# Performance work log

Hardware: AMD Instinct MI355X
Metric: run time of the kernel (lower is better)

## Reference

```python
import jax, jax.numpy as jnp
import numpy as np
import math

N = 4096; NFEAT = 512; HID = 128; H = 4; DH = HID // H; NC = 16; FF = 2 * HID


def _ln(x, g, b):
    m = jnp.mean(x, -1, keepdims=True)
    v = jnp.var(x, -1, keepdims=True)
    return (x - m) / jnp.sqrt(v + 1e-5) * g + b


def setup_inputs() -> dict:
    key = jax.random.key(0)
    ks = jax.random.split(key, 16)

    def w(k, shape):
        s = 1.0 / np.sqrt(shape[0])
        return jax.random.uniform(k, shape, jnp.float32, -s, s)

    inp = {}
    inp['e'] = jax.random.uniform(ks[0], (N,), jnp.float32, 0.0, 2.0)  # eigenvalues
    inp['u'] = jax.random.normal(ks[1], (N, N), jnp.float32) / np.sqrt(N)  # eigenvectors
    inp['x'] = jax.random.normal(ks[2], (N, NFEAT), jnp.float32)
    # feat_encoder: Linear(nfeat,hid) -> ReLU -> Linear(hid,nclass)
    inp['fe_w1'] = w(ks[3], (NFEAT, HID)); inp['fe_b1'] = jnp.zeros((HID,), jnp.float32)
    inp['fe_w2'] = w(ks[4], (HID, NC));    inp['fe_b2'] = jnp.zeros((NC,), jnp.float32)
    # eig_w: Linear(hid+1, hid)
    inp['ew_w'] = w(ks[5], (HID + 1, HID)); inp['ew_b'] = jnp.zeros((HID,), jnp.float32)
    inp['ln1_g'] = jnp.ones((HID,), jnp.float32); inp['ln1_b'] = jnp.zeros((HID,), jnp.float32)
    # custom MHA projections
    inp['wq'] = w(ks[6], (HID, HID)); inp['bq'] = jnp.zeros((HID,), jnp.float32)
    inp['wk'] = w(ks[7], (HID, HID)); inp['bk'] = jnp.zeros((HID,), jnp.float32)
    inp['wv'] = w(ks[8], (HID, HID)); inp['bv'] = jnp.zeros((HID,), jnp.float32)
    inp['wo'] = w(ks[9], (HID, HID)); inp['bo'] = jnp.zeros((HID,), jnp.float32)
    inp['ln2_g'] = jnp.ones((HID,), jnp.float32); inp['ln2_b'] = jnp.zeros((HID,), jnp.float32)
    # FFN with GELU
    inp['ffn_w1'] = w(ks[10], (HID, FF)); inp['ffn_b1'] = jnp.zeros((FF,), jnp.float32)
    inp['ffn_w2'] = w(ks[11], (FF, HID)); inp['ffn_b2'] = jnp.zeros((HID,), jnp.float32)
    # decoder: Linear(hid, nheads)
    inp['dec_w'] = w(ks[12], (HID, H)); inp['dec_b'] = jnp.zeros((H,), jnp.float32)
    # SpecLayer weight (norm='none' -> ones, [1, nheads+1, nclass])
    inp['spec_w'] = jnp.ones((1, H + 1, NC), jnp.float32)
    return inp


def reference(e, u, x, fe_w1, fe_b1, fe_w2, fe_b2, ew_w, ew_b, ln1_g, ln1_b,
              wq, bq, wk, bk, wv, bv, wo, bo, ln2_g, ln2_b,
              ffn_w1, ffn_b1, ffn_w2, ffn_b2, dec_w, dec_b, spec_w):
    n = e.shape[0]
    # feat_encoder (norm='none' path), dropout is identity at p=0
    h = jax.nn.relu(x @ fe_w1 + fe_b1) @ fe_w2 + fe_b2  # [N, NC]
    # SineEncoding
    div = jnp.exp(jnp.arange(0, HID, 2, dtype=jnp.float32) * (-math.log(10000.0) / HID))  # [HID/2]
    pe = (e * 100.0)[:, None] * div                     # [N, HID/2]
    sc = jnp.concatenate([jnp.sin(pe), jnp.cos(pe)], axis=1)   # [N, HID] (sin_cos_encoding)
    eeig = jnp.concatenate([e[:, None], sc], axis=1)           # [N, HID+1]
    eigw = eeig @ ew_w + ew_b                                  # [N, HID]
    # Custom multi-head attention with dot-product relative-position bias
    m = _ln(eigw, ln1_g, ln1_b)
    q = (m @ wq + bq).reshape(n, H, DH).transpose(1, 0, 2)     # [H, N, DH]
    k = (m @ wk + bk).reshape(n, H, DH).transpose(1, 0, 2)
    v = (m @ wv + bv).reshape(n, H, DH).transpose(1, 0, 2)
    rel = sc @ sc.T                                            # [N, N]
    scale = 1.0 / math.sqrt(DH)
    scores = jnp.einsum('hnd,hmd->hnm', q, k) * scale + rel[None] * scale  # [H, N, N]
    attn = jax.nn.softmax(scores, axis=-1)
    out = jnp.einsum('hnm,hmd->hnd', attn, v).transpose(1, 0, 2).reshape(n, HID)
    out = out @ wo + bo
    eig = eigw + out
    f = _ln(eig, ln2_g, ln2_b)
    f = jax.nn.gelu(f @ ffn_w1 + ffn_b1, approximate=False) @ ffn_w2 + ffn_b2
    eig = eig + f
    new_e = eig @ dec_w + dec_b                                # [N, H]
    # Spectral propagation (single SpecLayer, norm='none')
    utx = u.T @ h                                              # [N, NC]
    scaled = new_e.T[:, :, None] * utx[None]                   # [H, N, NC]
    props = jnp.einsum('nm,hmc->hnc', u, scaled)               # [H, N, NC]
    bf = jnp.concatenate([h[:, None, :], props.transpose(1, 0, 2)], axis=1)  # [N, H+1, NC]
    return jnp.sum(bf * spec_w, axis=1)                        # [N, NC]
```

## Files before the change

kernel.cpp:

```cpp
#include <hip/hip_runtime.h>
#include <math.h>

#define N 4096
#define NFEAT 512
#define HID 128
#define NHEAD 4
#define DH 32
#define NC 16
#define FF 256
#define NSPLIT 32
#define NCHUNK 8

typedef _Float16 f16;
typedef unsigned int uint;
typedef _Float16 f16x8 __attribute__((ext_vector_type(8)));
typedef _Float16 f16x2 __attribute__((ext_vector_type(2)));
typedef float f32x16 __attribute__((ext_vector_type(16)));

#define SCALE 0.17677669529663687f
#define LOG2E 1.44269504088896f
#define SH2   (-14.0f * 1.44269504088896f)

__global__ __launch_bounds__(256) void k_feat(const float* __restrict__ x,
    const float* __restrict__ w1, const float* __restrict__ b1,
    const float* __restrict__ w2, const float* __restrict__ b2,
    float* __restrict__ h) {
  __shared__ float xs[8][NFEAT];
  __shared__ float h1s[8][HID];
  int r0 = blockIdx.x * 8, tid = threadIdx.x;
  for (int i = tid; i < 8 * (NFEAT / 4); i += 256) {
    int rr = i >> 7, c4 = i & 127;
    ((float4*)xs[rr])[c4] = *(const float4*)(x + (size_t)(r0 + rr) * NFEAT + c4 * 4);
  }
  __syncthreads();
  int c = tid & 127, rb = tid >> 7;
  float acc[4];
#pragma unroll
  for (int i = 0; i < 4; ++i) acc[i] = b1[c];
  for (int k2 = 0; k2 < NFEAT; ++k2) {
    float wv = w1[k2 * HID + c];
#pragma unroll
    for (int i = 0; i < 4; ++i) acc[i] += xs[rb + 2 * i][k2] * wv;
  }
#pragma unroll
  for (int i = 0; i < 4; ++i) h1s[rb + 2 * i][c] = fmaxf(acc[i], 0.f);
  __syncthreads();
  if (tid < 128) {
    int rr = tid >> 4, cc = tid & 15;
    float a2 = b2[cc];
    for (int k2 = 0; k2 < HID; ++k2)
      a2 += h1s[rr][k2] * w2[k2 * NC + cc];
    h[(size_t)(r0 + rr) * NC + cc] = a2;
  }
}

__global__ __launch_bounds__(256) void k_sine_eigw(const float* __restrict__ e,
    const float* __restrict__ eww, const float* __restrict__ ewb,
    f16* __restrict__ sc_h, f16* __restrict__ scS_h, float* __restrict__ eigw) {
  __shared__ float scs[8][HID];
  __shared__ float es[8];
  int r0 = blockIdx.x * 8, tid = threadIdx.x;
  if (tid < 8) es[tid] = e[r0 + tid];
  __syncthreads();
  for (int i = tid; i < 8 * 64; i += 256) {
    int rr = i >> 6, j = i & 63;
    float div = expf((float)(2 * j) * (-0.07195578415606394f));
    float pe = es[rr] * 100.0f * div;
    scs[rr][j]      = sinf(pe);
    scs[rr][j + 64] = cosf(pe);
  }
  __syncthreads();
  for (int i = tid; i < 8 * 64; i += 256) {
    int rr = i >> 6, jj = i & 63;
    float x0 = scs[rr][2 * jj], x1 = scs[rr][2 * jj + 1];
    f16x2 a; a[0] = (f16)x0; a[1] = (f16)x1;
    f16x2 b; b[0] = (f16)(x0 * SCALE); b[1] = (f16)(x1 * SCALE);
    ((f16x2*)sc_h)[(size_t)(r0 + rr) * 64 + jj] = a;
    ((f16x2*)scS_h)[(size_t)(r0 + rr) * 64 + jj] = b;
  }
  int c = tid & 127, rb = tid >> 7;
  float acc[4];
#pragma unroll
  for (int i = 0; i < 4; ++i) acc[i] = ewb[c] + es[rb + 2 * i] * eww[c];
  for (int k2 = 0; k2 < HID; ++k2) {
    float wv = eww[(1 + k2) * HID + c];
#pragma unroll
    for (int i = 0; i < 4; ++i) acc[i] += scs[rb + 2 * i][k2] * wv;
  }
#pragma unroll
  for (int i = 0; i < 4; ++i)
    eigw[(size_t)(r0 + rb + 2 * i) * HID + c] = acc[i];
}

__global__ __launch_bounds__(256) void k_ln(const float* __restrict__ in,
    const float* __restrict__ g, const float* __restrict__ b, float* __restrict__ out) {
  int row = blockIdx.x * 4 + (threadIdx.x >> 6);
  int l = threadIdx.x & 63;
  float2 v2 = *(const float2*)(in + (size_t)row * HID + l * 2);
  float s = v2.x + v2.y;
  float ss = v2.x * v2.x + v2.y * v2.y;
#pragma unroll
  for (int off = 32; off > 0; off >>= 1) {
    s  += __shfl_down(s, off, 64);
    ss += __shfl_down(ss, off, 64);
  }
  s = __shfl(s, 0, 64); ss = __shfl(ss, 0, 64);
  float mean = s * (1.0f / HID);
  float var = ss * (1.0f / HID) - mean * mean;
  float inv = 1.0f / sqrtf(var + 1e-5f);
  float2 g2 = *(const float2*)(g + l * 2);
  float2 b2 = *(const float2*)(b + l * 2);
  float2 o;
  o.x = (v2.x - mean) * inv * g2.x + b2.x;
  o.y = (v2.y - mean) * inv * g2.y + b2.y;
  *(float2*)(out + (size_t)row * HID + l * 2) = o;
}

template <bool RES, bool F16O>
__global__ __launch_bounds__(256) void k_lin128(const float* __restrict__ in,
    const float* __restrict__ w, const float* __restrict__ bias,
    const float* __restrict__ res, float* __restrict__ out, f16* __restrict__ outh,
    float oscale) {
  __shared__ float as[8][HID];
  int r0 = blockIdx.x * 8, tid = threadIdx.x;
  {
    int rr = tid >> 5, c4 = tid & 31;
    ((float4*)as[rr])[c4] = *(const float4*)(in + (size_t)(r0 + rr) * HID + c4 * 4);
  }
  __syncthreads();
  int c = tid & 127, rb = tid >> 7;
  float acc[4];
#pragma unroll
  for (int i = 0; i < 4; ++i) acc[i] = bias[c];
  for (int k2 = 0; k2 < HID; ++k2) {
    float wv = w[k2 * HID + c];
#pragma unroll
    for (int i = 0; i < 4; ++i) acc[i] += as[rb + 2 * i][k2] * wv;
  }
#pragma unroll
  for (int i = 0; i < 4; ++i) {
    int rr = rb + 2 * i;
    float o = acc[i];
    if (RES) o += res[(size_t)(r0 + rr) * HID + c];
    if (F16O) outh[(size_t)(r0 + rr) * HID + c] = (f16)(o * oscale);
    else      out[(size_t)(r0 + rr) * HID + c] = o;
  }
}

__global__ __launch_bounds__(256) void k_vT(const float* __restrict__ v, f16* __restrict__ vT) {
  int n0 = blockIdx.x * 64, d0 = blockIdx.y * 32, tid = threadIdx.x;
  int d = tid & 31;
#pragma unroll
  for (int it = 0; it < 4; ++it) {
    int j = (tid >> 5) + it * 8;
    float x0 = v[(size_t)(n0 + 2 * j) * HID + d0 + d];
    float x1 = v[(size_t)(n0 + 2 * j + 1) * HID + d0 + d];
    f16x2 hh; hh[0] = (f16)x0; hh[1] = (f16)x1;
    ((f16x2*)vT)[((size_t)(d0 + d) * N + n0) / 2 + j] = hh;
  }
}

__global__ __launch_bounds__(256) void k_attn2(const f16* __restrict__ qh, const f16* __restrict__ kh,
    const f16* __restrict__ vTh, const f16* __restrict__ sch, const f16* __restrict__ scSh,
    float* __restrict__ pacc, float* __restrict__ pl) {
  int tid = threadIdx.x, h = tid >> 6, lane = tid & 63, lrow = lane & 31, lhalf = lane >> 5;
  int n0 = blockIdx.x * 32, ntile = blockIdx.x, chunk = blockIdx.y;
  const f16* qp = qh + (size_t)(n0 + lrow) * HID + 32 * h + lhalf * 8;
  f16x8 qb0 = *(const f16x8*)(qp);
  f16x8 qb1 = *(const f16x8*)(qp + 16);
  f16x8 bsc[8];
#pragma unroll
  for (int ks = 0; ks < 8; ++ks)
    bsc[ks] = *(const f16x8*)(sch + (size_t)(n0 + lrow) * HID + ks * 16 + lhalf * 8);
  f32x16 oacc = {0,0,0,0,0,0,0,0,0,0,0,0,0,0,0,0};
  float l = 0.f;
  for (int mt = 0; mt < 16; ++mt) {
    int m0 = chunk * 512 + mt * 32;
    const f16* kp = kh + (size_t)(m0 + lrow) * HID + 32 * h + lhalf * 8;
    f16x8 ka0 = *(const f16x8*)(kp);
    f16x8 ka1 = *(const f16x8*)(kp + 16);
    const f16* vp = vTh + (size_t)(32 * h + lrow) * N + m0 + lhalf * 8;
    f16x8 va0 = *(const f16x8*)(vp);
    f16x8 va1 = *(const f16x8*)(vp + 16);
    f32x16 sacc = {0,0,0,0,0,0,0,0,0,0,0,0,0,0,0,0};
#pragma unroll
    for (int ks = 0; ks < 8; ++ks) {
      f16x8 as = *(const f16x8*)(scSh + (size_t)(m0 + lrow) * HID + ks * 16 + lhalf * 8);
      sacc = __builtin_amdgcn_mfma_f32_32x32x16_f16(as, bsc[ks], sacc, 0, 0, 0);
    }
    sacc = __builtin_amdgcn_mfma_f32_32x32x16_f16(ka0, qb0, sacc, 0, 0, 0);
    sacc = __builtin_amdgcn_mfma_f32_32x32x16_f16(ka1, qb1, sacc, 0, 0, 0);
    uint w0[2], w1[2], w2[2], w3[2];
#pragma unroll
    for (int ks = 0; ks < 2; ++ks) {
      float p[8];
#pragma unroll
      for (int i = 0; i < 8; ++i)
        p[i] = exp2f(fmaf(sacc[ks * 8 + i], LOG2E, SH2));
      uint Wa = __builtin_bit_cast(uint, __builtin_amdgcn_cvt_pkrtz(p[0], p[1]));
      uint Wb = __builtin_bit_cast(uint, __builtin_amdgcn_cvt_pkrtz(p[2], p[3]));
      uint Wc = __builtin_bit_cast(uint, __builtin_amdgcn_cvt_pkrtz(p[4], p[5]));
      uint Wd = __builtin_bit_cast(uint, __builtin_amdgcn_cvt_pkrtz(p[6], p[7]));
      {
        f16x2 ha = __builtin_bit_cast(f16x2, Wa), hb = __builtin_bit_cast(f16x2, Wb);
        f16x2 hc = __builtin_bit_cast(f16x2, Wc), hd = __builtin_bit_cast(f16x2, Wd);
        l += (float)ha[0] + (float)ha[1] + (float)hb[0] + (float)hb[1]
           + (float)hc[0] + (float)hc[1] + (float)hd[0] + (float)hd[1];
      }
      uint Wax = (uint)__shfl_xor((int)Wa, 32, 64);
      uint Wbx = (uint)__shfl_xor((int)Wb, 32, 64);
      uint Wcx = (uint)__shfl_xor((int)Wc, 32, 64);
      uint Wdx = (uint)__shfl_xor((int)Wd, 32, 64);
      bool hi = (lhalf != 0);
      w0[ks] = hi ? Wcx : Wa;
      w1[ks] = hi ? Wdx : Wb;
      w2[ks] = hi ? Wc : Wax;
      w3[ks] = hi ? Wd : Wbx;
    }
    f16x8 pb0 = __builtin_bit_cast(f16x8, make_uint4(w0[0], w1[0], w2[0], w3[0]));
    f16x8 pb1 = __builtin_bit_cast(f16x8, make_uint4(w0[1], w1[1], w2[1], w3[1]));
    oacc = __builtin_amdgcn_mfma_f32_32x32x16_f16(va0, pb0, oacc, 0, 0, 0);
    oacc = __builtin_amdgcn_mfma_f32_32x32x16_f16(va1, pb1, oacc, 0, 0, 0);
  }
  l += __shfl_xor(l, 32, 64);
  float* pp = pacc + ((size_t)(chunk * 4 + h) * 128 + ntile) * 1024 + lane * 16;
  *(float4*)(pp +  0) = make_float4(oacc[0],  oacc[1],  oacc[2],  oacc[3]);
  *(float4*)(pp +  4) = make_float4(oacc[4],  oacc[5],  oacc[6],  oacc[7]);
  *(float4*)(pp +  8) = make_float4(oacc[8],  oacc[9],  oacc[10], oacc[11]);
  *(float4*)(pp + 12) = make_float4(oacc[12], oacc[13], oacc[14], oacc[15]);
  if (lane < 32) pl[(size_t)(chunk * 4 + h) * N + n0 + lrow] = l;
}

__global__ __launch_bounds__(256) void k_attn_merge2(const float* __restrict__ pacc,
    const float* __restrict__ pl, float* __restrict__ attno) {
  __shared__ float ao[32][132];
  int tid = threadIdx.x, h = tid >> 6, lane = tid & 63, lrow = lane & 31, lhalf = lane >> 5;
  int ntile = blockIdx.x, n0 = ntile * 32;
  float o[16];
#pragma unroll
  for (int r = 0; r < 16; ++r) o[r] = 0.f;
  float l = 0.f;
#pragma unroll
  for (int c = 0; c < NCHUNK; ++c) {
    const float* pp = pacc + ((size_t)(c * 4 + h) * 128 + ntile) * 1024 + lane * 16;
    float4 r0 = *(const float4*)(pp), r1 = *(const float4*)(pp + 4);
    float4 r2 = *(const float4*)(pp + 8), r3 = *(const float4*)(pp + 12);
    o[0]+=r0.x; o[1]+=r0.y; o[2]+=r0.z; o[3]+=r0.w;
    o[4]+=r1.x; o[5]+=r1.y; o[6]+=r1.z; o[7]+=r1.w;
    o[8]+=r2.x; o[9]+=r2.y; o[10]+=r2.z; o[11]+=r2.w;
    o[12]+=r3.x; o[13]+=r3.y; o[14]+=r3.z; o[15]+=r3.w;
    l += pl[(size_t)(c * 4 + h) * N + n0 + lrow];
  }
  float inv = 1.0f / l;
#pragma unroll
  for (int r = 0; r < 16; ++r) {
    int d = (r & 3) + 8 * (r >> 2) + 4 * lhalf;
    ao[lrow][h * 32 + d] = o[r] * inv;
  }
  __syncthreads();
  for (int i = tid; i < 32 * 32; i += 256) {
    int row = i >> 5, c4 = i & 31;
    *(float4*)(attno + (size_t)(n0 + row) * HID + c4 * 4) = *(float4*)&ao[row][c4 * 4];
  }
}

__global__ __launch_bounds__(256) void k_ffn(const float* __restrict__ fln,
    const float* __restrict__ w1, const float* __restrict__ b1,
    const float* __restrict__ w2, const float* __restrict__ b2,
    const float* __restrict__ eig, float* __restrict__ out) {
  __shared__ float fs[8][HID];
  __shared__ float t1[8][FF];
  int r0 = blockIdx.x * 8, tid = threadIdx.x;
  {
    int rr = tid >> 5, c4 = tid & 31;
    ((float4*)fs[rr])[c4] = *(const float4*)(fln + (size_t)(r0 + rr) * HID + c4 * 4);
  }
  __syncthreads();
  {
    float acc[8];
#pragma unroll
    for (int i = 0; i < 8; ++i) acc[i] = b1[tid];
    for (int k2 = 0; k2 < HID; ++k2) {
      float wv = w1[k2 * FF + tid];
#pragma unroll
      for (int i = 0; i < 8; ++i) acc[i] += fs[i][k2] * wv;
    }
#pragma unroll
    for (int i = 0; i < 8; ++i) {
      float xg = acc[i];
      t1[i][tid] = 0.5f * xg * (1.0f + erff(xg * 0.7071067811865476f));
    }
  }
  __syncthreads();
  int c = tid & 127, rb = tid >> 7;
  float acc2[4];
#pragma unroll
  for (int i = 0; i < 4; ++i) acc2[i] = b2[c];
  for (int k2 = 0; k2 < FF; ++k2) {
    float wv = w2[k2 * HID + c];
#pragma unroll
    for (int i = 0; i < 4; ++i) acc2[i] += t1[rb + 2 * i][k2] * wv;
  }
#pragma unroll
  for (int i = 0; i < 4; ++i) {
    int rr = r0 + rb + 2 * i;
    out[(size_t)rr * HID + c] = acc2[i] + eig[(size_t)rr * HID + c];
  }
}

__global__ __launch_bounds__(256) void k_dec(const float* __restrict__ eig2,
    const float* __restrict__ dw, const float* __restrict__ db, float* __restrict__ newe) {
  int tid = threadIdx.x;
  int r = tid >> 4, j = (tid >> 2) & 3, q = tid & 3;
  int n = blockIdx.x * 16 + r;
  const float* ep = eig2 + (size_t)n * HID + q * 32;
  float a = 0.f;
#pragma unroll
  for (int t4 = 0; t4 < 8; ++t4) {
    float4 e4 = *(const float4*)(ep + t4 * 4);
    int k0 = q * 32 + t4 * 4;
    a += e4.x * dw[k0 * NHEAD + j] + e4.y * dw[(k0 + 1) * NHEAD + j]
       + e4.z * dw[(k0 + 2) * NHEAD + j] + e4.w * dw[(k0 + 3) * NHEAD + j];
  }
  a += __shfl_down(a, 1, 64);
  a += __shfl_down(a, 2, 64);
  if (q == 0) newe[n * NHEAD + j] = db[j] + a;
}

__global__ __launch_bounds__(256) void k_utx(const float* __restrict__ u,
    const float* __restrict__ h, float* __restrict__ putx) {
  __shared__ float hs[128][NC];
  int tid = threadIdx.x;
  int m = blockIdx.x * 256 + tid;
  int n0 = blockIdx.y * 128;
  for (int i = tid; i < 128 * 4; i += 256) {
    int row = i >> 2, cq = i & 3;
    ((float4*)hs[row])[cq] = *(const float4*)(h + (size_t)(n0 + row) * NC + cq * 4);
  }
  __syncthreads();
  float acc[16];
#pragma unroll
  for (int c = 0; c < 16; ++c) acc[c] = 0.f;
  for (int nb = 0; nb < 16; ++nb) {
    float uv[8];
#pragma unroll
    for (int t = 0; t < 8; ++t)
      uv[t] = u[(size_t)(n0 + nb * 8 + t) * N + m];
#pragma unroll
    for (int t = 0; t < 8; ++t) {
      int nl = nb * 8 + t;
      float4 h0 = ((const float4*)hs[nl])[0];
      float4 h1 = ((const float4*)hs[nl])[1];
      float4 h2 = ((const float4*)hs[nl])[2];
      float4 h3 = ((const float4*)hs[nl])[3];
      acc[0]  += uv[t] * h0.x;  acc[1]  += uv[t] * h0.y;
      acc[2]  += uv[t] * h0.z;  acc[3]  += uv[t] * h0.w;
      acc[4]  += uv[t] * h1.x;  acc[5]  += uv[t] * h1.y;
      acc[6]  += uv[t] * h1.z;  acc[7]  += uv[t] * h1.w;
      acc[8]  += uv[t] * h2.x;  acc[9]  += uv[t] * h2.y;
      acc[10] += uv[t] * h2.z;  acc[11] += uv[t] * h2.w;
      acc[12] += uv[t] * h3.x;  acc[13] += uv[t] * h3.y;
      acc[14] += uv[t] * h3.z;  acc[15] += uv[t] * h3.w;
    }
  }
  float* o = putx + ((size_t)blockIdx.y * N + m) * NC;
  *(float4*)(o +  0) = make_float4(acc[0],  acc[1],  acc[2],  acc[3]);
  *(float4*)(o +  4) = make_float4(acc[4],  acc[5],  acc[6],  acc[7]);
  *(float4*)(o +  8) = make_float4(acc[8],  acc[9],  acc[10], acc[11]);
  *(float4*)(o + 12) = make_float4(acc[12], acc[13], acc[14], acc[15]);
}

__global__ __launch_bounds__(256) void k_sbuild(const float* __restrict__ putx,
    const float* __restrict__ newe, const float* __restrict__ specw,
    float* __restrict__ sT) {
  int i = blockIdx.x * 256 + threadIdx.x;
  int m = i >> 2, cq = i & 3;
  float4 t = make_float4(0.f, 0.f, 0.f, 0.f);
#pragma unroll 8
  for (int ch = 0; ch < NSPLIT; ++ch) {
    float4 p = *(const float4*)(putx + ((size_t)ch * N + m) * NC + cq * 4);
    t.x += p.x; t.y += p.y; t.z += p.z; t.w += p.w;
  }
  float4 ne = *(const float4*)(newe + (size_t)m * NHEAD);
  float fac[4];
#pragma unroll
  for (int cc = 0; cc < 4; ++cc) {
    int c = cq * 4 + cc;
    fac[cc] = ne.x * specw[1 * NC + c] + ne.y * specw[2 * NC + c]
            + ne.z * specw[3 * NC + c] + ne.w * specw[4 * NC + c];
  }
  sT[(size_t)(cq * 4 + 0) * N + m] = t.x * fac[0];
  sT[(size_t)(cq * 4 + 1) * N + m] = t.y * fac[1];
  sT[(size_t)(cq * 4 + 2) * N + m] = t.z * fac[2];
  sT[(size_t)(cq * 4 + 3) * N + m] = t.w * fac[3];
}

__global__ __launch_bounds__(256) void k_final(const float* __restrict__ u,
    const float* __restrict__ sT, float* __restrict__ pfin) {
  __shared__ float sTl[16][256];
  int tid = threadIdx.x, w = tid >> 6, lane = tid & 63;
  int r0 = blockIdx.x * 16;
  size_t mbase = (size_t)blockIdx.y * 2048;
  float a[4][16];
#pragma unroll
  for (int r = 0; r < 4; ++r)
#pragma unroll
    for (int c = 0; c < 16; ++c) a[r][c] = 0.f;
  for (int chunk = 0; chunk < 8; ++chunk) {
    size_t mc0 = mbase + chunk * 256;
    __syncthreads();
    for (int i = tid; i < 16 * 64; i += 256) {
      int c = i >> 6, q = i & 63;
      ((float4*)&sTl[c][0])[q] = *(const float4*)(sT + (size_t)c * N + mc0 + q * 4);
    }
    __syncthreads();
    float4 u4[4];
#pragma unroll
    for (int r = 0; r < 4; ++r)
      u4[r] = *(const float4*)(u + (size_t)(r0 + w * 4 + r) * N + mc0 + 4 * lane);
#pragma unroll
    for (int c = 0; c < 16; ++c) {
      float4 sv = *(const float4*)&sTl[c][4 * lane];
#pragma unroll
      for (int r = 0; r < 4; ++r)
        a[r][c] += u4[r].x * sv.x + u4[r].y * sv.y + u4[r].z * sv.z + u4[r].w * sv.w;
    }
  }
#pragma unroll
  for (int off = 32; off > 0; off >>= 1)
#pragma unroll
    for (int r = 0; r < 4; ++r)
#pragma unroll
      for (int c = 0; c < 16; ++c)
        a[r][c] += __shfl_xor(a[r][c], off, 64);
  if (lane == 0) {
#pragma unroll
    for (int r = 0; r < 4; ++r) {
      float* op = pfin + ((size_t)blockIdx.y * N + r0 + w * 4 + r) * NC;
      *(float4*)(op +  0) = make_float4(a[r][0],  a[r][1],  a[r][2],  a[r][3]);
      *(float4*)(op +  4) = make_float4(a[r][4],  a[r][5],  a[r][6],  a[r][7]);
      *(float4*)(op +  8) = make_float4(a[r][8],  a[r][9],  a[r][10], a[r][11]);
      *(float4*)(op + 12) = make_float4(a[r][12], a[r][13], a[r][14], a[r][15]);
    }
  }
}

__global__ __launch_bounds__(256) void k_finmerge(const float* __restrict__ pfin,
    const float* __restrict__ h, const float* __restrict__ specw, float* __restrict__ out) {
  int i = blockIdx.x * 256 + threadIdx.x;
  int n = i >> 2, cq = i & 3;
  float4 f0 = *(const float4*)(pfin + (size_t)n * NC + cq * 4);
  float4 f1 = *(const float4*)(pfin + ((size_t)N + n) * NC + cq * 4);
  float4 h4 = *(const float4*)(h + (size_t)n * NC + cq * 4);
  int c0 = cq * 4;
  float4 o;
  o.x = f0.x + f1.x + h4.x * specw[c0 + 0];
  o.y = f0.y + f1.y + h4.y * specw[c0 + 1];
  o.z = f0.z + f1.z + h4.z * specw[c0 + 2];
  o.w = f0.w + f1.w + h4.w * specw[c0 + 3];
  *(float4*)(out + (size_t)n * NC + cq * 4) = o;
}

extern "C" void kernel_launch(void* const* d_in, const int* in_sizes, int n_in,
                              void* d_out, int out_size, void* d_ws, size_t ws_size,
                              hipStream_t stream) {
  const float* e    = (const float*)d_in[0];
  const float* u    = (const float*)d_in[1];
  const float* x    = (const float*)d_in[2];
  const float* few1 = (const float*)d_in[3];
  const float* feb1 = (const float*)d_in[4];
  const float* few2 = (const float*)d_in[5];
  const float* feb2 = (const float*)d_in[6];
  const float* eww  = (const float*)d_in[7];
  const float* ewb  = (const float*)d_in[8];
  const float* ln1g = (const float*)d_in[9];
  const float* ln1b = (const float*)d_in[10];
  const float* wq   = (const float*)d_in[11];
  const float* bq   = (const float*)d_in[12];
  const float* wk   = (const float*)d_in[13];
  const float* bk   = (const float*)d_in[14];
  const float* wv_  = (const float*)d_in[15];
  const float* bv   = (const float*)d_in[16];
  const float* wo   = (const float*)d_in[17];
  const float* bo   = (const float*)d_in[18];
  const float* ln2g = (const float*)d_in[19];
  const float* ln2b = (const float*)d_in[20];
  const float* fw1  = (const float*)d_in[21];
  const float* fb1  = (const float*)d_in[22];
  const float* fw2  = (const float*)d_in[23];
  const float* fb2  = (const float*)d_in[24];
  const float* dw   = (const float*)d_in[25];
  const float* db   = (const float*)d_in[26];
  const float* spw  = (const float*)d_in[27];
  float* out = (float*)d_out;

  char* wsb = (char*)d_ws;
  auto alloc = [&](size_t bytes) { char* p = wsb; wsb += (bytes + 1023) & ~(size_t)1023; return p; };
  float* h    = (float*)alloc(N * NC * 4);
  f16*  sc_h  = (f16*)alloc(N * HID * 2);
  f16*  scS_h = (f16*)alloc(N * HID * 2);
  float* eigw = (float*)alloc(N * HID * 4);
  float* mln  = (float*)alloc(N * HID * 4);
  f16*  q_h   = (f16*)alloc(N * HID * 2);
  f16*  k_h   = (f16*)alloc(N * HID * 2);
  float* v    = (float*)alloc(N * HID * 4);
  f16*  vT_h  = (f16*)alloc(N * HID * 2);
  float* attno= (float*)alloc(N * HID * 4);
  float* eig  = (float*)alloc(N * HID * 4);
  float* fln  = (float*)alloc(N * HID * 4);
  float* eig2 = (float*)alloc(N * HID * 4);
  float* newe = (float*)alloc(N * NHEAD * 4);
  float* sT   = (float*)alloc((size_t)NC * N * 4);
  float* putx = (float*)alloc((size_t)NSPLIT * N * NC * 4);
  float* pacc = (float*)alloc((size_t)NCHUNK * 4 * 128 * 1024 * 4);
  float* pl   = (float*)alloc((size_t)NCHUNK * 4 * N * 4);
  float* pfin = (float*)alloc((size_t)2 * N * NC * 4);

  k_feat<<<N / 8, 256, 0, stream>>>(x, few1, feb1, few2, feb2, h);
  k_utx<<<dim3(N / 256, NSPLIT), 256, 0, stream>>>(u, h, putx);
  k_sine_eigw<<<N / 8, 256, 0, stream>>>(e, eww, ewb, sc_h, scS_h, eigw);
  k_ln<<<N / 4, 256, 0, stream>>>(eigw, ln1g, ln1b, mln);
  k_lin128<false, true><<<N / 8, 256, 0, stream>>>(mln, wq, bq, nullptr, nullptr, q_h, SCALE);
  k_lin128<false, true><<<N / 8, 256, 0, stream>>>(mln, wk, bk, nullptr, nullptr, k_h, 1.0f);
  k_lin128<false, false><<<N / 8, 256, 0, stream>>>(mln, wv_, bv, nullptr, v, nullptr, 1.0f);
  k_vT<<<dim3(N / 64, 4), 256, 0, stream>>>(v, vT_h);
  k_attn2<<<dim3(128, NCHUNK), 256, 0, stream>>>(q_h, k_h, vT_h, sc_h, scS_h, pacc, pl);
  k_attn_merge2<<<128, 256, 0, stream>>>(pacc, pl, attno);
  k_lin128<true, false><<<N / 8, 256, 0, stream>>>(attno, wo, bo, eigw, eig, nullptr, 1.0f);
  k_ln<<<N / 4, 256, 0, stream>>>(eig, ln2g, ln2b, fln);
  k_ffn<<<N / 8, 256, 0, stream>>>(fln, fw1, fb1, fw2, fb2, eig, eig2);
  k_dec<<<N / 16, 256, 0, stream>>>(eig2, dw, db, newe);
  k_sbuild<<<N * 4 / 256, 256, 0, stream>>>(putx, newe, spw, sT);
  k_final<<<dim3(N / 16, 2), 256, 0, stream>>>(u, sT, pfin);
  k_finmerge<<<N * 4 / 256, 256, 0, stream>>>(pfin, h, spw, out);
}
```

Before: 418.8 us.

## Share rel-bias tile computation across heads via LDS in attention kernel

Before, each of the four waves (one per head) recomputed the same sc·scᵀ relative-bias tile with 8 MFMAs per 32-key tile. Now each wave computes the bias for a different 32-key tile of a 128-key group and writes it to shared memory. After a barrier, all waves read the four tiles and add their own QK contribution, which cuts the redundant bias MFMAs by a factor of four. The trade is two block barriers per group plus LDS traffic, and launch bounds now request 4 blocks per CU, which may constrain registers.

```diff
diff --git a/kernel.cpp b/kernel.cpp
--- a/kernel.cpp
+++ b/kernel.cpp
@@ -10,6 +10,8 @@
 #define FF 256
 #define NSPLIT 32
 #define NCHUNK 8
+#define CHUNKM (N / NCHUNK)
+#define NGRP (CHUNKM / 128)
 
 typedef _Float16 f16;
 typedef unsigned int uint;
@@ -160,75 +162,98 @@
   }
 }
 
-__global__ __launch_bounds__(256) void k_attn2(const f16* __restrict__ qh, const f16* __restrict__ kh,
+__global__ __launch_bounds__(256, 4) void k_attn2(const f16* __restrict__ qh, const f16* __restrict__ kh,
     const f16* __restrict__ vTh, const f16* __restrict__ sch, const f16* __restrict__ scSh,
     float* __restrict__ pacc, float* __restrict__ pl) {
-  int tid = threadIdx.x, h = tid >> 6, lane = tid & 63, lrow = lane & 31, lhalf = lane >> 5;
+  __shared__ float relbuf[4 * 4 * 64 * 4];
+  int tid = threadIdx.x, w = tid >> 6, lane = tid & 63, lrow = lane & 31, lhalf = lane >> 5;
   int n0 = blockIdx.x * 32, ntile = blockIdx.x, chunk = blockIdx.y;
-  const f16* qp = qh + (size_t)(n0 + lrow) * HID + 32 * h + lhalf * 8;
+  const f16* qp = qh + (size_t)(n0 + lrow) * HID + 32 * w + lhalf * 8;
   f16x8 qb0 = *(const f16x8*)(qp);
   f16x8 qb1 = *(const f16x8*)(qp + 16);
-  f16x8 bsc[8];
-#pragma unroll
-  for (int ks = 0; ks < 8; ++ks)
-    bsc[ks] = *(const f16x8*)(sch + (size_t)(n0 + lrow) * HID + ks * 16 + lhalf * 8);
   f32x16 oacc = {0,0,0,0,0,0,0,0,0,0,0,0,0,0,0,0};
   float l = 0.f;
-  for (int mt = 0; mt < 16; ++mt) {
-    int m0 = chunk * 512 + mt * 32;
-    const f16* kp = kh + (size_t)(m0 + lrow) * HID + 32 * h + lhalf * 8;
-    f16x8 ka0 = *(const f16x8*)(kp);
-    f16x8 ka1 = *(const f16x8*)(kp + 16);
-    const f16* vp = vTh + (size_t)(32 * h + lrow) * N + m0 + lhalf * 8;
-    f16x8 va0 = *(const f16x8*)(vp);
-    f16x8 va1 = *(const f16x8*)(vp + 16);
-    f32x16 sacc = {0,0,0,0,0,0,0,0,0,0,0,0,0,0,0,0};
+  for (int g = 0; g < NGRP; ++g) {
+    int m0my = chunk * CHUNKM + (g * 4 + w) * 32;
+    f32x16 rs = {0,0,0,0,0,0,0,0,0,0,0,0,0,0,0,0};
 #pragma unroll
     for (int ks = 0; ks < 8; ++ks) {
-      f16x8 as = *(const f16x8*)(scSh + (size_t)(m0 + lrow) * HID + ks * 16 + lhalf * 8);
-      sacc = __builtin_amdgcn_mfma_f32_32x32x16_f16(as, bsc[ks], sacc, 0, 0, 0);
-    }
-    sacc = __builtin_amdgcn_mfma_f32_32x32x16_f16(ka0, qb0, sacc, 0, 0, 0);
-    sacc = __builtin_amdgcn_mfma_f32_32x32x16_f16(ka1, qb1, sacc, 0, 0, 0);
-    uint w0[2], w1[2], w2[2], w3[2];
-#pragma unroll
-    for (int ks = 0; ks < 2; ++ks) {
-      float p[8];
-#pragma unroll
-      for (int i = 0; i < 8; ++i)
-        p[i] = exp2f(fmaf(sacc[ks * 8 + i], LOG2E, SH2));
-      uint Wa = __builtin_bit_cast(uint, __builtin_amdgcn_cvt_pkrtz(p[0], p[1]));
-      uint Wb = __builtin_bit_cast(uint, __builtin_amdgcn_cvt_pkrtz(p[2], p[3]));
-      uint Wc = __builtin_bit_cast(uint, __builtin_amdgcn_cvt_pkrtz(p[4], p[5]));
-      uint Wd = __builtin_bit_cast(uint, __builtin_amdgcn_cvt_pkrtz(p[6], p[7]));
+      f16x8 as = *(const f16x8*)(scSh + (size_t)(m0my + lrow) * HID + ks * 16 + lhalf * 8);
+      f16x8 bs = *(const f16x8*)(sch + (size_t)(n0 + lrow) * HID + ks * 16 + lhalf * 8);
+      rs = __builtin_amdgcn_mfma_f32_32x32x16_f16(as, bs, rs, 0, 0, 0);
+    }
+    __syncthreads();
+    {
+      int base = w * 1024 + lane * 4;
+      *(float4*)&relbuf[base +   0] = make_float4(rs[0],  rs[1],  rs[2],  rs[3]);
+      *(float4*)&relbuf[base + 256] = make_float4(rs[4],  rs[5],  rs[6],  rs[7]);
+      *(float4*)&relbuf[base + 512] = make_float4(rs[8],  rs[9],  rs[10], rs[11]);
+      *(float4*)&relbuf[base + 768] = make_float4(rs[12], rs[13], rs[14], rs[15]);
+    }
+    __syncthreads();
+#pragma unroll
+    for (int t = 0; t < 4; ++t) {
+      int m0 = chunk * CHUNKM + (g * 4 + t) * 32;
+      f32x16 sacc;
       {
-        f16x2 ha = __builtin_bit_cast(f16x2, Wa), hb = __builtin_bit_cast(f16x2, Wb);
-        f16x2 hc = __builtin_bit_cast(f16x2, Wc), hd = __builtin_bit_cast(f16x2, Wd);
-        l += (float)ha[0] + (float)ha[1] + (float)hb[0] + (float)hb[1]
-           + (float)hc[0] + (float)hc[1] + (float)hd[0] + (float)hd[1];
+        int base = t * 1024 + lane * 4;
+        float4 r0 = *(const float4*)&relbuf[base +   0];
+        float4 r1 = *(const float4*)&relbuf[base + 256];
+        float4 r2 = *(const float4*)&relbuf[base + 512];
+        float4 r3 = *(const float4*)&relbuf[base + 768];
+        sacc[0]=r0.x;  sacc[1]=r0.y;  sacc[2]=r0.z;  sacc[3]=r0.w;
+        sacc[4]=r1.x;  sacc[5]=r1.y;  sacc[6]=r1.z;  sacc[7]=r1.w;
+        sacc[8]=r2.x;  sacc[9]=r2.y;  sacc[10]=r2.z; sacc[11]=r2.w;
+        sacc[12]=r3.x; sacc[13]=r3.y; sacc[14]=r3.z; sacc[15]=r3.w;
       }
-      uint Wax = (uint)__shfl_xor((int)Wa, 32, 64);
-      uint Wbx = (uint)__shfl_xor((int)Wb, 32, 64);
-      uint Wcx = (uint)__shfl_xor((int)Wc, 32, 64);
-      uint Wdx = (uint)__shfl_xor((int)Wd, 32, 64);
-      bool hi = (lhalf != 0);
-      w0[ks] = hi ? Wcx : Wa;
-      w1[ks] = hi ? Wdx : Wb;
-      w2[ks] = hi ? Wc : Wax;
-      w3[ks] = hi ? Wd : Wbx;
-    }
-    f16x8 pb0 = __builtin_bit_cast(f16x8, make_uint4(w0[0], w1[0], w2[0], w3[0]));
-    f16x8 pb1 = __builtin_bit_cast(f16x8, make_uint4(w0[1], w1[1], w2[1], w3[1]));
-    oacc = __builtin_amdgcn_mfma_f32_32x32x16_f16(va0, pb0, oacc, 0, 0, 0);
-    oacc = __builtin_amdgcn_mfma_f32_32x32x16_f16(va1, pb1, oacc, 0, 0, 0);
+      const f16* kp = kh + (size_t)(m0 + lrow) * HID + 32 * w + lhalf * 8;
+      f16x8 ka0 = *(const f16x8*)(kp);
+      f16x8 ka1 = *(const f16x8*)(kp + 16);
+      const f16* vp = vTh + (size_t)(32 * w + lrow) * N + m0 + lhalf * 8;
+      f16x8 va0 = *(const f16x8*)(vp);
+      f16x8 va1 = *(const f16x8*)(vp + 16);
+      sacc = __builtin_amdgcn_mfma_f32_32x32x16_f16(ka0, qb0, sacc, 0, 0, 0);
+      sacc = __builtin_amdgcn_mfma_f32_32x32x16_f16(ka1, qb1, sacc, 0, 0, 0);
+      uint w0[2], w1[2], w2[2], w3[2];
+#pragma unroll
+      for (int ks = 0; ks < 2; ++ks) {
+        float p[8];
+#pragma unroll
+        for (int i = 0; i < 8; ++i)
+          p[i] = exp2f(fmaf(sacc[ks * 8 + i], LOG2E, SH2));
+        uint Wa = __builtin_bit_cast(uint, __builtin_amdgcn_cvt_pkrtz(p[0], p[1]));
+        uint Wb = __builtin_bit_cast(uint, __builtin_amdgcn_cvt_pkrtz(p[2], p[3]));
+        uint Wc = __builtin_bit_cast(uint, __builtin_amdgcn_cvt_pkrtz(p[4], p[5]));
+        uint Wd = __builtin_bit_cast(uint, __builtin_amdgcn_cvt_pkrtz(p[6], p[7]));
+        {
+          f16x2 ha = __builtin_bit_cast(f16x2, Wa), hb = __builtin_bit_cast(f16x2, Wb);
+          f16x2 hc = __builtin_bit_cast(f16x2, Wc), hd = __builtin_bit_cast(f16x2, Wd);
+          l += (float)ha[0] + (float)ha[1] + (float)hb[0] + (float)hb[1]
+             + (float)hc[0] + (float)hc[1] + (float)hd[0] + (float)hd[1];
+        }
+        uint Wax = (uint)__shfl_xor((int)Wa, 32, 64);
+        uint Wbx = (uint)__shfl_xor((int)Wb, 32, 64);
+        uint Wcx = (uint)__shfl_xor((int)Wc, 32, 64);
+        uint Wdx = (uint)__shfl_xor((int)Wd, 32, 64);
+        bool hi = (lhalf != 0);
+        w0[ks] = hi ? Wcx : Wa;
+        w1[ks] = hi ? Wdx : Wb;
+        w2[ks] = hi ? Wc : Wax;
+        w3[ks] = hi ? Wd : Wbx;
+      }
+      f16x8 pb0 = __builtin_bit_cast(f16x8, make_uint4(w0[0], w1[0], w2[0], w3[0]));
+      f16x8 pb1 = __builtin_bit_cast(f16x8, make_uint4(w0[1], w1[1], w2[1], w3[1]));
+      oacc = __builtin_amdgcn_mfma_f32_32x32x16_f16(va0, pb0, oacc, 0, 0, 0);
+      oacc = __builtin_amdgcn_mfma_f32_32x32x16_f16(va1, pb1, oacc, 0, 0, 0);
+    }
   }
   l += __shfl_xor(l, 32, 64);
-  float* pp = pacc + ((size_t)(chunk * 4 + h) * 128 + ntile) * 1024 + lane * 16;
+  float* pp = pacc + ((size_t)(chunk * 4 + w) * 128 + ntile) * 1024 + lane * 16;
   *(float4*)(pp +  0) = make_float4(oacc[0],  oacc[1],  oacc[2],  oacc[3]);
   *(float4*)(pp +  4) = make_float4(oacc[4],  oacc[5],  oacc[6],  oacc[7]);
   *(float4*)(pp +  8) = make_float4(oacc[8],  oacc[9],  oacc[10], oacc[11]);
   *(float4*)(pp + 12) = make_float4(oacc[12], oacc[13], oacc[14], oacc[15]);
-  if (lane < 32) pl[(size_t)(chunk * 4 + h) * N + n0 + lrow] = l;
+  if (lane < 32) pl[(size_t)(chunk * 4 + w) * N + n0 + lrow] = l;
 }
 
 __global__ __launch_bounds__(256) void k_attn_merge2(const float* __restrict__ pacc,
```

After: 378.0 us. -9.7%, faster.
